# Kernel optimization log

Measured on AMD Instinct MI355X. Metric: run time of the kernel, lower is better.

## Reference

```python
import jax, jax.numpy as jnp
import numpy as np

B, S, H, NH, I, V, P, T = 8, 512, 768, 12, 3072, 30522, 512, 2
D = H // NH
EPS = 1e-12


def _ln(x, g, b):
    m = x.mean(-1, keepdims=True)
    v = ((x - m) ** 2).mean(-1, keepdims=True)
    return (x - m) / jnp.sqrt(v + EPS) * g + b


def setup_inputs() -> dict:
    key = jax.random.key(0)
    ks = jax.random.split(key, 24)
    s = 0.02
    f32 = jnp.float32
    d = {
        'x': jax.random.randint(ks[0], (B, S), 0, V, dtype=jnp.int32),
        'W_word': (jax.random.normal(ks[1], (V, H)) * s).astype(f32),
        'W_pos': (jax.random.normal(ks[2], (P, H)) * s).astype(f32),
        'W_type': (jax.random.normal(ks[3], (T, H)) * s).astype(f32),
        'g_emb': jnp.ones((H,), f32), 'b_emb': jnp.zeros((H,), f32),
        'Wq': (jax.random.normal(ks[4], (H, H)) * s).astype(f32), 'bq': jnp.zeros((H,), f32),
        'Wk': (jax.random.normal(ks[5], (H, H)) * s).astype(f32), 'bk': jnp.zeros((H,), f32),
        'Wv': (jax.random.normal(ks[6], (H, H)) * s).astype(f32), 'bv': jnp.zeros((H,), f32),
        'Wo': (jax.random.normal(ks[7], (H, H)) * s).astype(f32), 'bo': jnp.zeros((H,), f32),
        'g_attn': jnp.ones((H,), f32), 'b_attn': jnp.zeros((H,), f32),
        'Wi': (jax.random.normal(ks[8], (H, I)) * s).astype(f32), 'bi': jnp.zeros((I,), f32),
        'Wd': (jax.random.normal(ks[9], (I, H)) * s).astype(f32), 'bd': jnp.zeros((H,), f32),
        'g_out': jnp.ones((H,), f32), 'b_out': jnp.zeros((H,), f32),
        'Wp': (jax.random.normal(ks[10], (H, H)) * s).astype(f32), 'bp': jnp.zeros((H,), f32),
    }
    return d


def _forward(x, W_word, W_pos, W_type, g_emb, b_emb, Wq, bq, Wk, bk, Wv, bv,
             Wo, bo, g_attn, b_attn, Wi, bi, Wd, bd, g_out, b_out, Wp, bp):
    # embeddings: word + position(arange) + token_type(all zeros -> row 0)
    h = W_word[x] + W_pos[jnp.arange(S)][None, :, :] + W_type[0][None, None, :]
    h = _ln(h, g_emb, b_emb)
    scale = 1.0 / jnp.sqrt(jnp.float32(D))
    # NOTE: the torch module shares one set of layer weights across all 6 layers.
    for _ in range(6):
        q = (h @ Wq + bq).reshape(B, S, NH, D).transpose(0, 2, 1, 3)  # bhsd
        k = (h @ Wk + bk).reshape(B, S, NH, D).transpose(0, 2, 1, 3)
        v = (h @ Wv + bv).reshape(B, S, NH, D).transpose(0, 2, 1, 3)
        scores = jnp.einsum('bhqd,bhkd->bhqk', q, k) * scale
        probs = jax.nn.softmax(scores, axis=-1)
        ctx = jnp.einsum('bhqk,bhkd->bhqd', probs, v)
        ctx = ctx.transpose(0, 2, 1, 3).reshape(B, S, H)
        attn = ctx @ Wo + bo
        xa = _ln(h + attn, g_attn, b_attn)
        ff = jax.nn.gelu(xa @ Wi + bi, approximate=False) @ Wd + bd
        h = _ln(xa + ff, g_out, b_out)
    pooled = h[:, 0, :] @ Wp + bp  # no tanh in the original module
    return h, pooled


def reference(x, W_word, W_pos, W_type, g_emb, b_emb, Wq, bq, Wk, bk, Wv, bv,
              Wo, bo, g_attn, b_attn, Wi, bi, Wd, bd, g_out, b_out, Wp, bp):
    return _forward(x, W_word, W_pos, W_type, g_emb, b_emb, Wq, bq, Wk, bk, Wv, bv,
                    Wo, bo, g_attn, b_attn, Wi, bi, Wd, bd, g_out, b_out, Wp, bp)
```

## Files before the change

kernel.cpp:

```cpp
#include <hip/hip_runtime.h>
#include <hip/hip_bf16.h>
#include <math.h>

#define B_  8
#define S_  512
#define H_  768
#define NH_ 12
#define D_  64
#define I_  3072
#define NTOK (B_*S_)
#define LDQ 2304

typedef __attribute__((ext_vector_type(8))) __bf16 bf16x8;
typedef __attribute__((ext_vector_type(8))) unsigned short ushort8;
typedef __attribute__((ext_vector_type(4))) float  f32x4;

__device__ __forceinline__ float gelu_exact(float x) {
    return 0.5f * x * (1.0f + erff(x * 0.70710678118654752440f));
}

__device__ __forceinline__ unsigned short f2bf(float x) {
    __hip_bfloat16 h = __float2bfloat16(x);
    return *reinterpret_cast<unsigned short*>(&h);
}

__device__ __forceinline__ void gload16(const void* g, void* l) {
    __builtin_amdgcn_global_load_lds(
        (const __attribute__((address_space(1))) void*)g,
        (__attribute__((address_space(3))) void*)l,
        16, 0, 0);
}

#define SB0() __builtin_amdgcn_sched_barrier(0)

__global__ void cvtT_kernel(const float* __restrict__ W, __hip_bfloat16* __restrict__ WT,
                            int K, int N) {
    __shared__ float tile[32][33];
    int k0 = blockIdx.y * 32, n0 = blockIdx.x * 32;
    int tx = threadIdx.x & 31, ty = threadIdx.x >> 5;
    #pragma unroll
    for (int i = 0; i < 32; i += 8)
        tile[ty + i][tx] = W[(long)(k0 + ty + i) * N + n0 + tx];
    __syncthreads();
    #pragma unroll
    for (int i = 0; i < 32; i += 8)
        WT[(long)(n0 + ty + i) * K + k0 + tx] = __float2bfloat16(tile[tx][ty + i]);
}

__global__ void embed_ln_kernel(const int* __restrict__ ids,
                                const float* __restrict__ Wword,
                                const float* __restrict__ Wpos,
                                const float* __restrict__ Wtype,
                                const float* __restrict__ g,
                                const float* __restrict__ b,
                                float* __restrict__ out,
                                __hip_bfloat16* __restrict__ outb) {
    int t = blockIdx.x;
    int s = t % S_;
    long id = ids[t];
    int tid = threadIdx.x;
    float vals[3];
    float sum = 0.f, sq = 0.f;
    #pragma unroll
    for (int i = 0; i < 3; ++i) {
        int c = tid + 256 * i;
        float e = Wword[id * H_ + c] + Wpos[(long)s * H_ + c] + Wtype[c];
        vals[i] = e; sum += e; sq += e * e;
    }
    __shared__ float r1[256], r2[256];
    r1[tid] = sum; r2[tid] = sq; __syncthreads();
    for (int st = 128; st > 0; st >>= 1) {
        if (tid < st) { r1[tid] += r1[tid + st]; r2[tid] += r2[tid + st]; }
        __syncthreads();
    }
    float mean = r1[0] * (1.0f / H_);
    float var  = r2[0] * (1.0f / H_) - mean * mean;
    float inv  = rsqrtf(var + 1e-12f);
    #pragma unroll
    for (int i = 0; i < 3; ++i) {
        int c = tid + 256 * i;
        float v = (vals[i] - mean) * inv * g[c] + b[c];
        out[(long)t * H_ + c] = v;
        outb[(long)t * H_ + c] = __float2bfloat16(v);
    }
}

__global__ void add_ln_kernel(const float* __restrict__ a,
                              const float* __restrict__ r,
                              const float* __restrict__ g,
                              const float* __restrict__ bb,
                              float* __restrict__ out,
                              __hip_bfloat16* __restrict__ outb) {
    int t = blockIdx.x;
    int tid = threadIdx.x;
    float vals[3];
    float sum = 0.f, sq = 0.f;
    #pragma unroll
    for (int i = 0; i < 3; ++i) {
        int c = tid + 256 * i;
        float e = a[(long)t * H_ + c] + r[(long)t * H_ + c];
        vals[i] = e; sum += e; sq += e * e;
    }
    __shared__ float r1[256], r2[256];
    r1[tid] = sum; r2[tid] = sq; __syncthreads();
    for (int st = 128; st > 0; st >>= 1) {
        if (tid < st) { r1[tid] += r1[tid + st]; r2[tid] += r2[tid + st]; }
        __syncthreads();
    }
    float mean = r1[0] * (1.0f / H_);
    float var  = r2[0] * (1.0f / H_) - mean * mean;
    float inv  = rsqrtf(var + 1e-12f);
    #pragma unroll
    for (int i = 0; i < 3; ++i) {
        int c = tid + 256 * i;
        float v = (vals[i] - mean) * inv * g[c] + bb[c];
        out[(long)t * H_ + c] = v;
        outb[(long)t * H_ + c] = __float2bfloat16(v);
    }
}

__global__ void add_ln3_kernel(const float* __restrict__ a,
                               const float* __restrict__ r1p,
                               const float* __restrict__ r2p,
                               const float* __restrict__ g,
                               const float* __restrict__ bb,
                               float* __restrict__ out,
                               __hip_bfloat16* __restrict__ outb) {
    int t = blockIdx.x;
    int tid = threadIdx.x;
    float vals[3];
    float sum = 0.f, sq = 0.f;
    #pragma unroll
    for (int i = 0; i < 3; ++i) {
        int c = tid + 256 * i;
        float e = a[(long)t * H_ + c] + r1p[(long)t * H_ + c] + r2p[(long)t * H_ + c];
        vals[i] = e; sum += e; sq += e * e;
    }
    __shared__ float r1[256], r2[256];
    r1[tid] = sum; r2[tid] = sq; __syncthreads();
    for (int st = 128; st > 0; st >>= 1) {
        if (tid < st) { r1[tid] += r1[tid + st]; r2[tid] += r2[tid + st]; }
        __syncthreads();
    }
    float mean = r1[0] * (1.0f / H_);
    float var  = r2[0] * (1.0f / H_) - mean * mean;
    float inv  = rsqrtf(var + 1e-12f);
    #pragma unroll
    for (int i = 0; i < 3; ++i) {
        int c = tid + 256 * i;
        float v = (vals[i] - mean) * inv * g[c] + bb[c];
        out[(long)t * H_ + c] = v;
        outb[(long)t * H_ + c] = __float2bfloat16(v);
    }
}

template<int BM, int BN, int MI, int NJ, int ACT, int WF32, int WB16>
__global__ __launch_bounds__(256, 2) void mfma_gemm_kernel(
    const __hip_bfloat16* __restrict__ A,
    const __hip_bfloat16* __restrict__ BT,
    const float* __restrict__ bias,
    float* __restrict__ Cf,
    __hip_bfloat16* __restrict__ Cb,
    int M, int N, int Kc, int lda, int ldb) {
    constexpr int WC = BN / (NJ * 16);
    constexpr int WR = BM / (MI * 16);
    static_assert(WR * WC == 4, "4 waves");
    constexpr int LA = BM * 4 / 256;
    constexpr int LB = BN * 4 / 256;
    constexpr int L  = LA + LB;
    __shared__ __align__(16) __hip_bfloat16 sA[3][BM * 32];
    __shared__ __align__(16) __hip_bfloat16 sB[3][BN * 32];
    const int tid  = threadIdx.x;
    const int lane = tid & 63;
    const int w    = tid >> 6;
    const int wr   = w / WC, wc = w % WC;
    const int l15  = lane & 15, l4 = lane >> 4;
    const int m0 = blockIdx.y * BM, n0 = blockIdx.x * BN;
    const int koff = blockIdx.z * Kc;
    const int goff = (l15 >> 1) & 3;

    auto stage = [&](int buf, int k0) {
        #pragma unroll
        for (int t = 0; t < LA; ++t) {
            int c = tid + 256 * t;
            int row = c >> 2, gq = c & 3;
            int gsrc = gq ^ ((row >> 1) & 3);
            gload16(A + (long)(m0 + row) * lda + koff + k0 + gsrc * 8, &sA[buf][row * 32 + gq * 8]);
        }
        #pragma unroll
        for (int t = 0; t < LB; ++t) {
            int c = tid + 256 * t;
            int row = c >> 2, gq = c & 3;
            int gsrc = gq ^ ((row >> 1) & 3);
            gload16(BT + (long)(n0 + row) * ldb + koff + k0 + gsrc * 8, &sB[buf][row * 32 + gq * 8]);
        }
    };

    f32x4 acc[MI][NJ] = {};
    const int nk = Kc >> 5;

    stage(0, 0);
    if (nk > 1) stage(1, 32);
    for (int t = 0; t < nk; ++t) {
        const int cur = t % 3;
        if (t + 2 < nk) {
            stage((t + 2) % 3, (t + 2) * 32);
            asm volatile("s_waitcnt vmcnt(%0)" :: "i"(2 * L) : "memory");
        } else if (t + 1 < nk) {
            asm volatile("s_waitcnt vmcnt(%0)" :: "i"(L) : "memory");
        } else {
            asm volatile("s_waitcnt vmcnt(0)" ::: "memory");
        }
        SB0(); __builtin_amdgcn_s_barrier(); SB0();

        const int gsw = (l4 ^ goff) * 8;
        bf16x8 af[MI], bf[NJ];
        #pragma unroll
        for (int i = 0; i < MI; ++i)
            af[i] = *reinterpret_cast<const bf16x8*>(&sA[cur][(wr * MI * 16 + i * 16 + l15) * 32 + gsw]);
        #pragma unroll
        for (int j = 0; j < NJ; ++j)
            bf[j] = *reinterpret_cast<const bf16x8*>(&sB[cur][(wc * NJ * 16 + j * 16 + l15) * 32 + gsw]);
        #pragma unroll
        for (int i = 0; i < MI; ++i)
            #pragma unroll
            for (int j = 0; j < NJ; ++j)
                acc[i][j] = __builtin_amdgcn_mfma_f32_16x16x32_bf16(af[i], bf[j], acc[i][j], 0, 0, 0);

        SB0(); __builtin_amdgcn_s_barrier(); SB0();
    }

    float* Cfz = Cf + (size_t)blockIdx.z * M * N;
    #pragma unroll
    for (int i = 0; i < MI; ++i) {
        #pragma unroll
        for (int j = 0; j < NJ; ++j) {
            int col = n0 + wc * NJ * 16 + j * 16 + l15;
            float bv = bias[col];
            #pragma unroll
            for (int r = 0; r < 4; ++r) {
                int row = m0 + wr * MI * 16 + i * 16 + l4 * 4 + r;
                float v = acc[i][j][r] + bv;
                if (ACT == 1) v = gelu_exact(v);
                if (WF32) Cfz[(long)row * N + col] = v;
                if (WB16) Cb[(long)row * N + col] = __float2bfloat16(v);
            }
        }
    }
}

__global__ __launch_bounds__(256, 4) void flash_attn_kernel(
    const __hip_bfloat16* __restrict__ QKV,
    __hip_bfloat16* __restrict__ Ctx) {
    __shared__ __align__(16) unsigned short sK[64 * 72];
    __shared__ __align__(16) unsigned short sVt[64 * 72];
    __shared__ __align__(16) unsigned short sP[4 * 16 * 72];

    const int tid  = threadIdx.x;
    const int lane = tid & 63;
    const int w    = tid >> 6;
    const int l15  = lane & 15, l4 = lane >> 4;
    const int qb = blockIdx.x;
    const int bh = blockIdx.y;
    const int b  = bh / NH_, hd = bh % NH_;
    const long rbase = (long)b * S_ * LDQ;
    const int qoff = hd * D_, koff = H_ + hd * D_, voff = 2 * H_ + hd * D_;

    const int qrow0 = qb * 64 + w * 16;
    bf16x8 af[2];
    #pragma unroll
    for (int ks = 0; ks < 2; ++ks)
        af[ks] = *reinterpret_cast<const bf16x8*>(
            QKV + rbase + (long)(qrow0 + l15) * LDQ + qoff + ks * 32 + l4 * 8);

    f32x4 ctx[4] = {};
    float m_run[4], l_run[4];
    #pragma unroll
    for (int r = 0; r < 4; ++r) { m_run[r] = -1e30f; l_run[r] = 0.f; }

    const int sr = tid >> 2;
    const int sc = (tid & 3) * 16;
    unsigned short* pl = sP + w * (16 * 72);

    for (int kv0 = 0; kv0 < S_; kv0 += 64) {
        const __hip_bfloat16* kg = QKV + rbase + (long)(kv0 + sr) * LDQ + koff + sc;
        const __hip_bfloat16* vg = QKV + rbase + (long)(kv0 + sr) * LDQ + voff + sc;
        ushort8 kv_a = *reinterpret_cast<const ushort8*>(kg);
        ushort8 kv_b = *reinterpret_cast<const ushort8*>(kg + 8);
        ushort8 vv_a = *reinterpret_cast<const ushort8*>(vg);
        ushort8 vv_b = *reinterpret_cast<const ushort8*>(vg + 8);
        __syncthreads();
        *reinterpret_cast<ushort8*>(sK + sr * 72 + sc)     = kv_a;
        *reinterpret_cast<ushort8*>(sK + sr * 72 + sc + 8) = kv_b;
        #pragma unroll
        for (int i = 0; i < 8; ++i) {
            sVt[(sc + i) * 72 + sr]     = vv_a[i];
            sVt[(sc + 8 + i) * 72 + sr] = vv_b[i];
        }
        __syncthreads();

        f32x4 s[4];
        #pragma unroll
        for (int j = 0; j < 4; ++j) {
            s[j] = (f32x4){0.f, 0.f, 0.f, 0.f};
            #pragma unroll
            for (int ks = 0; ks < 2; ++ks) {
                bf16x8 bk = *reinterpret_cast<const bf16x8*>(sK + (j * 16 + l15) * 72 + ks * 32 + l4 * 8);
                s[j] = __builtin_amdgcn_mfma_f32_16x16x32_bf16(af[ks], bk, s[j], 0, 0, 0);
            }
        }
        #pragma unroll
        for (int j = 0; j < 4; ++j) s[j] *= 0.125f;

        #pragma unroll
        for (int r = 0; r < 4; ++r) {
            float mx = fmaxf(fmaxf(s[0][r], s[1][r]), fmaxf(s[2][r], s[3][r]));
            #pragma unroll
            for (int o = 1; o < 16; o <<= 1) mx = fmaxf(mx, __shfl_xor(mx, o));
            float mnew = fmaxf(m_run[r], mx);
            float sum = 0.f;
            #pragma unroll
            for (int j = 0; j < 4; ++j) {
                float p = __expf(s[j][r] - mnew);
                s[j][r] = p; sum += p;
            }
            #pragma unroll
            for (int o = 1; o < 16; o <<= 1) sum += __shfl_xor(sum, o);
            float resc = __expf(m_run[r] - mnew);
            l_run[r] = l_run[r] * resc + sum;
            m_run[r] = mnew;
            #pragma unroll
            for (int j = 0; j < 4; ++j) ctx[j][r] *= resc;
        }

        #pragma unroll
        for (int j = 0; j < 4; ++j)
            #pragma unroll
            for (int r = 0; r < 4; ++r)
                pl[(l4 * 4 + r) * 72 + j * 16 + l15] = f2bf(s[j][r]);

        #pragma unroll
        for (int ks = 0; ks < 2; ++ks) {
            bf16x8 ap = *reinterpret_cast<const bf16x8*>(pl + l15 * 72 + ks * 32 + l4 * 8);
            #pragma unroll
            for (int jd = 0; jd < 4; ++jd) {
                bf16x8 bv = *reinterpret_cast<const bf16x8*>(sVt + (jd * 16 + l15) * 72 + ks * 32 + l4 * 8);
                ctx[jd] = __builtin_amdgcn_mfma_f32_16x16x32_bf16(ap, bv, ctx[jd], 0, 0, 0);
            }
        }
    }

    #pragma unroll
    for (int r = 0; r < 4; ++r) {
        float inv = 1.f / l_run[r];
        long tok = (long)b * S_ + qb * 64 + w * 16 + l4 * 4 + r;
        #pragma unroll
        for (int jd = 0; jd < 4; ++jd)
            Ctx[tok * H_ + hd * D_ + jd * 16 + l15] = __float2bfloat16(ctx[jd][r] * inv);
    }
}

__global__ void pooled_kernel(const float* __restrict__ h,
                              const float* __restrict__ Wp,
                              const float* __restrict__ bp,
                              float* __restrict__ out) {
    int b = blockIdx.y;
    int col = blockIdx.x * 256 + threadIdx.x;
    const float* hb = h + (long)b * S_ * H_;
    float acc = 0.f;
    #pragma unroll 8
    for (int k = 0; k < H_; ++k)
        acc += hb[k] * Wp[(long)k * H_ + col];
    out[(long)b * H_ + col] = acc + bp[col];
}

extern "C" void kernel_launch(void* const* d_in, const int* in_sizes, int n_in,
                              void* d_out, int out_size, void* d_ws, size_t ws_size,
                              hipStream_t stream) {
    const int*   x      = (const int*)  d_in[0];
    const float* W_word = (const float*)d_in[1];
    const float* W_pos  = (const float*)d_in[2];
    const float* W_type = (const float*)d_in[3];
    const float* g_emb  = (const float*)d_in[4];
    const float* b_emb  = (const float*)d_in[5];
    const float* Wq     = (const float*)d_in[6];
    const float* bq     = (const float*)d_in[7];
    const float* Wk     = (const float*)d_in[8];
    const float* bk     = (const float*)d_in[9];
    const float* Wv     = (const float*)d_in[10];
    const float* bv     = (const float*)d_in[11];
    const float* Wo     = (const float*)d_in[12];
    const float* bo     = (const float*)d_in[13];
    const float* g_attn = (const float*)d_in[14];
    const float* b_attn = (const float*)d_in[15];
    const float* Wi     = (const float*)d_in[16];
    const float* bi     = (const float*)d_in[17];
    const float* Wd     = (const float*)d_in[18];
    const float* bd     = (const float*)d_in[19];
    const float* g_out  = (const float*)d_in[20];
    const float* b_out  = (const float*)d_in[21];
    const float* Wp     = (const float*)d_in[22];
    const float* bp     = (const float*)d_in[23];

    const size_t NT = (size_t)NTOK * H_;
    char* base = (char*)d_ws;
    size_t off = 0;
    auto alloc = [&](size_t bytes) -> char* {
        char* p = base + off;
        off += (bytes + 255) & ~(size_t)255;
        return p;
    };
    float* h    = (float*)alloc(NT * 4);
    float* xa   = (float*)alloc(NT * 4);
    float* kb   = (float*)alloc(NT * 4 * 2);
    float* kb2  = kb + NT;
    __hip_bfloat16* h_b   = (__hip_bfloat16*)alloc(NT * 2);
    __hip_bfloat16* xa_b  = (__hip_bfloat16*)alloc(NT * 2);
    __hip_bfloat16* qkv_b = (__hip_bfloat16*)alloc((size_t)NTOK * LDQ * 2);
    __hip_bfloat16* ctx_b = (__hip_bfloat16*)alloc(NT * 2);
    __hip_bfloat16* ff1_b = (__hip_bfloat16*)alloc((size_t)NTOK * I_ * 2);
    __hip_bfloat16* WqkvT = (__hip_bfloat16*)alloc((size_t)LDQ * H_ * 2);
    __hip_bfloat16* WoT = (__hip_bfloat16*)alloc((size_t)H_ * H_ * 2);
    __hip_bfloat16* WiT = (__hip_bfloat16*)alloc((size_t)H_ * I_ * 2);
    __hip_bfloat16* WdT = (__hip_bfloat16*)alloc((size_t)I_ * H_ * 2);
    float* bqkv = (float*)alloc(LDQ * 4);

    cvtT_kernel<<<dim3(H_/32, H_/32), 256, 0, stream>>>(Wq, WqkvT, H_, H_);
    cvtT_kernel<<<dim3(H_/32, H_/32), 256, 0, stream>>>(Wk, WqkvT + (size_t)H_ * H_, H_, H_);
    cvtT_kernel<<<dim3(H_/32, H_/32), 256, 0, stream>>>(Wv, WqkvT + (size_t)2 * H_ * H_, H_, H_);
    cvtT_kernel<<<dim3(H_/32, H_/32), 256, 0, stream>>>(Wo, WoT, H_, H_);
    cvtT_kernel<<<dim3(I_/32, H_/32), 256, 0, stream>>>(Wi, WiT, H_, I_);
    cvtT_kernel<<<dim3(H_/32, I_/32), 256, 0, stream>>>(Wd, WdT, I_, H_);
    hipMemcpyAsync(bqkv,          bq, H_ * 4, hipMemcpyDeviceToDevice, stream);
    hipMemcpyAsync(bqkv + H_,     bk, H_ * 4, hipMemcpyDeviceToDevice, stream);
    hipMemcpyAsync(bqkv + 2 * H_, bv, H_ * 4, hipMemcpyDeviceToDevice, stream);

    embed_ln_kernel<<<NTOK, 256, 0, stream>>>(x, W_word, W_pos, W_type, g_emb, b_emb, h, h_b);

    dim3 gqkv(LDQ/128, NTOK/256);
    dim3 gi(I_/128, NTOK/256);
    dim3 gff2(H_/128, NTOK/128, 2);
    dim3 g768(H_/64, NTOK/128);
    for (int layer = 0; layer < 6; ++layer) {
        mfma_gemm_kernel<256,128,8,4,0,0,1><<<gqkv, 256, 0, stream>>>(
            h_b, WqkvT, bqkv, nullptr, qkv_b, NTOK, LDQ, H_, H_, H_);
        flash_attn_kernel<<<dim3(S_/64, B_*NH_), 256, 0, stream>>>(qkv_b, ctx_b);
        mfma_gemm_kernel<128,64,4,2,0,1,0><<<g768, 256, 0, stream>>>(
            ctx_b, WoT, bo, kb, nullptr, NTOK, H_, H_, H_, H_);
        add_ln_kernel<<<NTOK, 256, 0, stream>>>(h, kb, g_attn, b_attn, xa, xa_b);
        mfma_gemm_kernel<256,128,8,4,1,0,1><<<gi, 256, 0, stream>>>(
            xa_b, WiT, bi, nullptr, ff1_b, NTOK, I_, H_, H_, H_);
        mfma_gemm_kernel<128,128,4,4,0,1,0><<<gff2, 256, 0, stream>>>(
            ff1_b, WdT, bd, kb, nullptr, NTOK, H_, I_/2, I_, I_);
        add_ln3_kernel<<<NTOK, 256, 0, stream>>>(xa, kb, kb2, g_out, b_out, h, h_b);
    }

    hipMemcpyAsync(d_out, h, NT * sizeof(float), hipMemcpyDeviceToDevice, stream);
    pooled_kernel<<<dim3(3, 8), 256, 0, stream>>>(h, Wp, bp, (float*)d_out + NT);
}
```

Baseline: 1.219 ms.

## Replace 4-wave block GEMM with single-wave 64x64 tile GEMM kernel

Replaces the 256-thread multi-wave GEMM (large 256x128/128x128 tiles, triple-buffered, block barriers) with a one-wave 64x64 tile kernel that double-buffers through LDS and needs no block-wide barriers. Each tile refills as soon as its fragments are read into registers. The output projection becomes a split-K launch, and its two partial sums are merged in add_ln3. Bias is added only in the z=0 split. This removes barrier synchronisation and gives many more blocks, but each tile reuses less data, so global and LDS traffic per FLOP rise. The shallower two-stage prefetch may also hide memory latency less well.

```diff
diff --git a/kernel.cpp b/kernel.cpp
--- a/kernel.cpp
+++ b/kernel.cpp
@@ -154,92 +154,82 @@
     }
 }
 
-template<int BM, int BN, int MI, int NJ, int ACT, int WF32, int WB16>
-__global__ __launch_bounds__(256, 2) void mfma_gemm_kernel(
+template<int ACT, int WF32, int WB16>
+__global__ __launch_bounds__(64, 2) void wave_gemm_kernel(
     const __hip_bfloat16* __restrict__ A,
     const __hip_bfloat16* __restrict__ BT,
     const float* __restrict__ bias,
     float* __restrict__ Cf,
     __hip_bfloat16* __restrict__ Cb,
     int M, int N, int Kc, int lda, int ldb) {
-    constexpr int WC = BN / (NJ * 16);
-    constexpr int WR = BM / (MI * 16);
-    static_assert(WR * WC == 4, "4 waves");
-    constexpr int LA = BM * 4 / 256;
-    constexpr int LB = BN * 4 / 256;
-    constexpr int L  = LA + LB;
-    __shared__ __align__(16) __hip_bfloat16 sA[3][BM * 32];
-    __shared__ __align__(16) __hip_bfloat16 sB[3][BN * 32];
-    const int tid  = threadIdx.x;
-    const int lane = tid & 63;
-    const int w    = tid >> 6;
-    const int wr   = w / WC, wc = w % WC;
+    __shared__ __align__(16) unsigned short sA[2][64 * 32];
+    __shared__ __align__(16) unsigned short sB[2][64 * 32];
+    const int lane = threadIdx.x;
     const int l15  = lane & 15, l4 = lane >> 4;
-    const int m0 = blockIdx.y * BM, n0 = blockIdx.x * BN;
+    const int m0 = blockIdx.y * 64, n0 = blockIdx.x * 64;
     const int koff = blockIdx.z * Kc;
     const int goff = (l15 >> 1) & 3;
 
     auto stage = [&](int buf, int k0) {
         #pragma unroll
-        for (int t = 0; t < LA; ++t) {
-            int c = tid + 256 * t;
+        for (int u = 0; u < 4; ++u) {
+            int c = u * 64 + lane;
             int row = c >> 2, gq = c & 3;
             int gsrc = gq ^ ((row >> 1) & 3);
-            gload16(A + (long)(m0 + row) * lda + koff + k0 + gsrc * 8, &sA[buf][row * 32 + gq * 8]);
-        }
-        #pragma unroll
-        for (int t = 0; t < LB; ++t) {
-            int c = tid + 256 * t;
+            gload16(A + (long)(m0 + row) * lda + koff + k0 + gsrc * 8, &sA[buf][c * 8]);
+        }
+        #pragma unroll
+        for (int u = 0; u < 4; ++u) {
+            int c = u * 64 + lane;
             int row = c >> 2, gq = c & 3;
             int gsrc = gq ^ ((row >> 1) & 3);
-            gload16(BT + (long)(n0 + row) * ldb + koff + k0 + gsrc * 8, &sB[buf][row * 32 + gq * 8]);
+            gload16(BT + (long)(n0 + row) * ldb + koff + k0 + gsrc * 8, &sB[buf][c * 8]);
         }
     };
 
-    f32x4 acc[MI][NJ] = {};
+    f32x4 acc[4][4] = {};
     const int nk = Kc >> 5;
 
     stage(0, 0);
     if (nk > 1) stage(1, 32);
     for (int t = 0; t < nk; ++t) {
-        const int cur = t % 3;
-        if (t + 2 < nk) {
-            stage((t + 2) % 3, (t + 2) * 32);
-            asm volatile("s_waitcnt vmcnt(%0)" :: "i"(2 * L) : "memory");
-        } else if (t + 1 < nk) {
-            asm volatile("s_waitcnt vmcnt(%0)" :: "i"(L) : "memory");
-        } else {
-            asm volatile("s_waitcnt vmcnt(0)" ::: "memory");
-        }
-        SB0(); __builtin_amdgcn_s_barrier(); SB0();
+        const int cur = t & 1;
+        if (t + 1 < nk) asm volatile("s_waitcnt vmcnt(8)" ::: "memory");
+        else            asm volatile("s_waitcnt vmcnt(0)" ::: "memory");
+        SB0();
 
         const int gsw = (l4 ^ goff) * 8;
-        bf16x8 af[MI], bf[NJ];
-        #pragma unroll
-        for (int i = 0; i < MI; ++i)
-            af[i] = *reinterpret_cast<const bf16x8*>(&sA[cur][(wr * MI * 16 + i * 16 + l15) * 32 + gsw]);
-        #pragma unroll
-        for (int j = 0; j < NJ; ++j)
-            bf[j] = *reinterpret_cast<const bf16x8*>(&sB[cur][(wc * NJ * 16 + j * 16 + l15) * 32 + gsw]);
-        #pragma unroll
-        for (int i = 0; i < MI; ++i)
-            #pragma unroll
-            for (int j = 0; j < NJ; ++j)
+        bf16x8 af[4], bf[4];
+        #pragma unroll
+        for (int i = 0; i < 4; ++i)
+            af[i] = *reinterpret_cast<const bf16x8*>(&sA[cur][(i * 16 + l15) * 32 + gsw]);
+        #pragma unroll
+        for (int j = 0; j < 4; ++j)
+            bf[j] = *reinterpret_cast<const bf16x8*>(&sB[cur][(j * 16 + l15) * 32 + gsw]);
+
+        asm volatile("s_waitcnt lgkmcnt(0)" ::: "memory");
+        SB0();
+        if (t + 2 < nk) stage(cur, (t + 2) * 32);
+        SB0();
+
+        #pragma unroll
+        for (int i = 0; i < 4; ++i)
+            #pragma unroll
+            for (int j = 0; j < 4; ++j)
                 acc[i][j] = __builtin_amdgcn_mfma_f32_16x16x32_bf16(af[i], bf[j], acc[i][j], 0, 0, 0);
-
-        SB0(); __builtin_amdgcn_s_barrier(); SB0();
     }
 
     float* Cfz = Cf + (size_t)blockIdx.z * M * N;
-    #pragma unroll
-    for (int i = 0; i < MI; ++i) {
-        #pragma unroll
-        for (int j = 0; j < NJ; ++j) {
-            int col = n0 + wc * NJ * 16 + j * 16 + l15;
-            float bv = bias[col];
+    const bool addb = (blockIdx.z == 0);
+    #pragma unroll
+    for (int i = 0; i < 4; ++i) {
+        #pragma unroll
+        for (int j = 0; j < 4; ++j) {
+            int col = n0 + j * 16 + l15;
+            float bv = addb ? bias[col] : 0.f;
             #pragma unroll
             for (int r = 0; r < 4; ++r) {
-                int row = m0 + wr * MI * 16 + i * 16 + l4 * 4 + r;
+                int row = m0 + i * 16 + l4 * 4 + r;
                 float v = acc[i][j][r] + bv;
                 if (ACT == 1) v = gelu_exact(v);
                 if (WF32) Cfz[(long)row * N + col] = v;
@@ -437,20 +427,20 @@
 
     embed_ln_kernel<<<NTOK, 256, 0, stream>>>(x, W_word, W_pos, W_type, g_emb, b_emb, h, h_b);
 
-    dim3 gqkv(LDQ/128, NTOK/256);
-    dim3 gi(I_/128, NTOK/256);
-    dim3 gff2(H_/128, NTOK/128, 2);
-    dim3 g768(H_/64, NTOK/128);
+    dim3 gqkv(LDQ/64, NTOK/64);
+    dim3 gi(I_/64, NTOK/64);
+    dim3 go(H_/64, NTOK/64, 2);
+    dim3 gff2(H_/64, NTOK/64, 2);
     for (int layer = 0; layer < 6; ++layer) {
-        mfma_gemm_kernel<256,128,8,4,0,0,1><<<gqkv, 256, 0, stream>>>(
+        wave_gemm_kernel<0,0,1><<<gqkv, 64, 0, stream>>>(
             h_b, WqkvT, bqkv, nullptr, qkv_b, NTOK, LDQ, H_, H_, H_);
         flash_attn_kernel<<<dim3(S_/64, B_*NH_), 256, 0, stream>>>(qkv_b, ctx_b);
-        mfma_gemm_kernel<128,64,4,2,0,1,0><<<g768, 256, 0, stream>>>(
-            ctx_b, WoT, bo, kb, nullptr, NTOK, H_, H_, H_, H_);
-        add_ln_kernel<<<NTOK, 256, 0, stream>>>(h, kb, g_attn, b_attn, xa, xa_b);
-        mfma_gemm_kernel<256,128,8,4,1,0,1><<<gi, 256, 0, stream>>>(
+        wave_gemm_kernel<0,1,0><<<go, 64, 0, stream>>>(
+            ctx_b, WoT, bo, kb, nullptr, NTOK, H_, H_/2, H_, H_);
+        add_ln3_kernel<<<NTOK, 256, 0, stream>>>(h, kb, kb2, g_attn, b_attn, xa, xa_b);
+        wave_gemm_kernel<1,0,1><<<gi, 64, 0, stream>>>(
             xa_b, WiT, bi, nullptr, ff1_b, NTOK, I_, H_, H_, H_);
-        mfma_gemm_kernel<128,128,4,4,0,1,0><<<gff2, 256, 0, stream>>>(
+        wave_gemm_kernel<0,1,0><<<gff2, 64, 0, stream>>>(
             ff1_b, WdT, bd, kb, nullptr, NTOK, H_, I_/2, I_, I_);
         add_ln3_kernel<<<NTOK, 256, 0, stream>>>(xa, kb, kb2, g_out, b_out, h, h_b);
     }
```

Result: slower. 1.368 ms (+12.2%).
